# Kernel optimization log

Hardware: AMD Instinct MI355X
Metric: run time of the kernel (lower is better)

## Reference

```python
import jax, jax.numpy as jnp
import numpy as np

N, E, F_IN, OUT = 10000, 80000, 128, 32
H1, C1 = 8, 256   # conv1: heads=8, out_channels=256, concat=True
H2, C2 = 1, OUT   # conv2: heads=1, out_channels=OUT, concat=False
NEG_SLOPE = 0.2


def _add_self_loops(edge_index, edge_attr, n_nodes):
    # PyG fill_value='mean': self-loop edge_attr = mean of incoming edge attrs per dst node
    src, dst = edge_index[0], edge_index[1]
    s = jax.ops.segment_sum(edge_attr, dst, num_segments=n_nodes)
    cnt = jax.ops.segment_sum(jnp.ones((edge_attr.shape[0],), edge_attr.dtype), dst, num_segments=n_nodes)
    self_attr = s / jnp.maximum(cnt, 1.0)[:, None]
    loop = jnp.arange(n_nodes)
    return (jnp.concatenate([src, loop]), jnp.concatenate([dst, loop]),
            jnp.concatenate([edge_attr, self_attr], axis=0))


def _gatv2(x, src, dst, edge_attr, Wl, bl, Wr, br, We, att, bias, heads, out_ch, concat, n_nodes):
    xl = (x @ Wl + bl).reshape(n_nodes, heads, out_ch)   # source-side projection
    xr = (x @ Wr + br).reshape(n_nodes, heads, out_ch)   # target-side projection
    e = (edge_attr @ We).reshape(-1, heads, out_ch)      # edge feature projection (no bias in PyG)
    m = jax.nn.leaky_relu(xl[src] + xr[dst] + e, NEG_SLOPE)   # [Etot, H, C]
    logits = jnp.einsum('ehc,hc->eh', m, att)            # per-edge attention logits
    # segment softmax over edges grouped by destination node (stable)
    lmax = jax.ops.segment_max(logits, dst, num_segments=n_nodes)
    ex = jnp.exp(logits - lmax[dst])
    denom = jax.ops.segment_sum(ex, dst, num_segments=n_nodes)
    alpha = ex / denom[dst]                              # [Etot, H]
    out = jax.ops.segment_sum(xl[src] * alpha[:, :, None], dst, num_segments=n_nodes)  # [N, H, C]
    out = out.reshape(n_nodes, heads * out_ch) if concat else out.mean(axis=1)
    return out + bias


def setup_inputs() -> dict:
    key = jax.random.key(0)
    ks = jax.random.split(key, 17)
    s = 0.05
    return {
        'x': jax.random.normal(ks[0], (N, F_IN), jnp.float32),
        'edge_index': jax.random.randint(ks[1], (2, E), 0, N),
        'edge_attr': jax.random.normal(ks[2], (E, F_IN), jnp.float32),
        # conv1 params
        'Wl1': jax.random.normal(ks[3], (F_IN, H1 * C1), jnp.float32) * s,
        'bl1': jnp.zeros((H1 * C1,), jnp.float32),
        'Wr1': jax.random.normal(ks[4], (F_IN, H1 * C1), jnp.float32) * s,
        'br1': jnp.zeros((H1 * C1,), jnp.float32),
        'We1': jax.random.normal(ks[5], (F_IN, H1 * C1), jnp.float32) * s,
        'att1': jax.random.normal(ks[6], (H1, C1), jnp.float32) * s,
        'b1': jnp.zeros((H1 * C1,), jnp.float32),
        # conv2 params (input dim = H1*C1 = 2048)
        'Wl2': jax.random.normal(ks[7], (H1 * C1, H2 * C2), jnp.float32) * s,
        'bl2': jnp.zeros((H2 * C2,), jnp.float32),
        'Wr2': jax.random.normal(ks[8], (H1 * C1, H2 * C2), jnp.float32) * s,
        'br2': jnp.zeros((H2 * C2,), jnp.float32),
        'We2': jax.random.normal(ks[9], (F_IN, H2 * C2), jnp.float32) * s,
        'att2': jax.random.normal(ks[10], (H2, C2), jnp.float32) * s,
        'b2': jnp.zeros((C2,), jnp.float32),
    }


def reference(x, edge_index, edge_attr, Wl1, bl1, Wr1, br1, We1, att1, b1,
              Wl2, bl2, Wr2, br2, We2, att2, b2):
    # mode='eval': all dropouts are identity
    src, dst, ea = _add_self_loops(edge_index, edge_attr, N)
    h = _gatv2(x, src, dst, ea, Wl1, bl1, Wr1, br1, We1, att1, b1, H1, C1, True, N)
    h = jax.nn.relu(h)
    out = _gatv2(h, src, dst, ea, Wl2, bl2, Wr2, br2, We2, att2, b2, H2, C2, False, N)
    return jax.nn.relu(out)
```

## Files before the change

kernel.cpp:

```cpp
#include <hip/hip_runtime.h>
#include <hip/hip_bf16.h>

#define N_NODES 10000
#define N_EDGES 80000
#define ETOT (N_EDGES + N_NODES)
#define FD 128
#define D1 2048
#define D2 32
#define NEG 0.2f

typedef __hip_bfloat16 bf16;
typedef __attribute__((ext_vector_type(8))) short short8;
typedef __attribute__((ext_vector_type(4))) short short4v;
typedef __attribute__((ext_vector_type(4))) float f32x4;

__device__ __forceinline__ bf16 f2b(float v){ return __float2bfloat16(v); }
__device__ __forceinline__ short f2bs(float v){ bf16 t=__float2bfloat16(v); return *(short*)&t; }
__device__ __forceinline__ float b2fs(short s){
    return __uint_as_float(((unsigned int)(unsigned short)s) << 16);
}

__global__ void k_deg(const int* __restrict__ ei, int* __restrict__ deg){
    int e = blockIdx.x*256 + threadIdx.x;
    if(e < N_EDGES) atomicAdd(&deg[ei[N_EDGES+e]], 1);
}

__global__ void k_scan(const int* __restrict__ deg, int* __restrict__ row_start){
    __shared__ int sdata[256];
    int tid = threadIdx.x;
    const int CH = 40;
    int base = tid*CH;
    int lsum = 0;
    for(int i=0;i<CH;i++){ int v=base+i; if(v<N_NODES) lsum += deg[v]+1; }
    sdata[tid]=lsum; __syncthreads();
    for(int off=1; off<256; off<<=1){
        int val = (tid>=off)? sdata[tid-off] : 0;
        __syncthreads();
        sdata[tid] += val;
        __syncthreads();
    }
    int run = (tid>0)? sdata[tid-1] : 0;
    for(int i=0;i<CH;i++){
        int v=base+i;
        if(v<=N_NODES){
            row_start[v]=run;
            if(v<N_NODES) run += deg[v]+1;
        }
    }
}

__global__ void k_fill(const int* __restrict__ ei, const int* __restrict__ row_start,
                       int* __restrict__ cursor, int* __restrict__ ecsr,
                       int* __restrict__ srcs, int* __restrict__ dsts){
    int e = blockIdx.x*256 + threadIdx.x;
    if(e >= ETOT) return;
    int src = (e < N_EDGES) ? ei[e]          : (e - N_EDGES);
    int dst = (e < N_EDGES) ? ei[N_EDGES+e]  : (e - N_EDGES);
    int p = atomicAdd(&cursor[dst], 1);
    int pos = row_start[dst]+p;
    ecsr[pos] = e;
    srcs[pos] = src;
    dsts[pos] = dst;
}

__global__ void k_selfmean(const int* __restrict__ ecsr, const int* __restrict__ row_start,
                           const float* __restrict__ ea, float* __restrict__ self_attr){
    int v = blockIdx.x, t = threadIdx.x;
    int start=row_start[v], end=row_start[v+1];
    float s=0.f; int cnt=0;
    for(int i=start;i<end;i++){
        int e=ecsr[i];
        if(e<N_EDGES){ s += ea[(size_t)e*FD+t]; cnt++; }
    }
    self_attr[(size_t)v*FD+t] = s / fmaxf((float)cnt, 1.f);
}

__global__ void k_packAll(const float* __restrict__ We1, const float* __restrict__ Wl1,
                          const float* __restrict__ Wr1, const float* __restrict__ Wl2,
                          const float* __restrict__ Wr2, const float* __restrict__ We2,
                          short* __restrict__ Wb1, short* __restrict__ Wbl1,
                          short* __restrict__ Wbr1, short* __restrict__ Wb2,
                          short* __restrict__ Wb2e){
    int y = blockIdx.y;
    int idx = blockIdx.x*256 + threadIdx.x;
    if(y < 3){
        const float* W = (y==0)? We1 : (y==1)? Wl1 : Wr1;
        short* Wb      = (y==0)? Wb1 : (y==1)? Wbl1 : Wbr1;
        int k = idx >> 11, c = idx & 2047;
        int cb = c>>4, col = c&15, kc = k>>5, quad = (k>>3)&3, j = k&7;
        Wb[((size_t)(cb*4+kc)*64 + quad*16 + col)*8 + j] = f2bs(W[idx]);
    } else {
        if(idx < 131072){
            int k = idx >> 6, c = idx & 63;
            float v = (c < 32) ? Wl2[k*32 + c] : Wr2[k*32 + (c-32)];
            int cb = c>>4, col = c&15, kc = k>>5, quad = (k>>3)&3, j = k&7;
            Wb2[((size_t)(cb*64+kc)*64 + quad*16 + col)*8 + j] = f2bs(v);
        } else if(idx < 131072+4096){
            int t = idx - 131072;
            int k = t >> 5, c = t & 31;
            int cb = c>>4, col = c&15, kc = k>>5, quad = (k>>3)&3, j = k&7;
            Wb2e[((size_t)(cb*4+kc)*64 + quad*16 + col)*8 + j] = f2bs(We2[t]);
        }
    }
}

__global__ __launch_bounds__(256) void k_gemm1m(const float* __restrict__ x,
        const short* __restrict__ Wbl, const float* __restrict__ bl, bf16* __restrict__ outl,
        const short* __restrict__ Wbr, const float* __restrict__ br, bf16* __restrict__ outr){
    const short* Wb   = (blockIdx.y==0)? Wbl : Wbr;
    const float* bias = (blockIdx.y==0)? bl  : br;
    bf16* outp        = (blockIdx.y==0)? outl: outr;
    __shared__ short a_lds[32*128];
    __shared__ float tile[4][32][20];
    int tid = threadIdx.x;
    int r0 = blockIdx.x*32;
    for(int q=tid; q<32*128; q+=256){
        int m=q>>7, k=q&127;
        int gr=r0+m;
        float v = (gr<N_NODES)? x[(size_t)gr*FD+k] : 0.f;
        int kc=k>>5, quad=(k>>3)&3, j=k&7;
        a_lds[((kc*4+quad)*32+m)*8+j] = f2bs(v);
    }
    __syncthreads();
    int w=tid>>6, lane=tid&63, quad=lane>>4, col=lane&15;
    int arow=lane&31, half=lane>>5;
    short8 af[2][4];
    #pragma unroll
    for(int mg=0;mg<2;mg++)
        #pragma unroll
        for(int kc=0;kc<4;kc++)
            af[mg][kc] = *(const short8*)&a_lds[((kc*4+quad)*32+mg*16+col)*8];
    int orow = r0 + arow;
    for(int cbl=0;cbl<32;cbl++){
        int cbg = w*32+cbl;
        f32x4 c0={0,0,0,0}, c1={0,0,0,0};
        #pragma unroll
        for(int kc=0;kc<4;kc++){
            short8 bfr = *(const short8*)(Wb + ((size_t)(cbg*4+kc)*64 + lane)*8);
            c0 = __builtin_amdgcn_mfma_f32_16x16x32_bf16(af[0][kc], bfr, c0, 0,0,0);
            c1 = __builtin_amdgcn_mfma_f32_16x16x32_bf16(af[1][kc], bfr, c1, 0,0,0);
        }
        #pragma unroll
        for(int rg=0;rg<4;rg++){
            tile[w][quad*4+rg][col]    = c0[rg];
            tile[w][16+quad*4+rg][col] = c1[rg];
        }
        int cg = cbg*16 + half*8;
        float4 t0 = *(float4*)&tile[w][arow][half*8];
        float4 t1 = *(float4*)&tile[w][arow][half*8+4];
        float4 b0 = *(const float4*)(bias+cg);
        float4 b1v = *(const float4*)(bias+cg+4);
        if(orow < N_NODES){
            float tv[8]={t0.x,t0.y,t0.z,t0.w,t1.x,t1.y,t1.z,t1.w};
            float bb[8]={b0.x,b0.y,b0.z,b0.w,b1v.x,b1v.y,b1v.z,b1v.w};
            short8 ov;
            #pragma unroll
            for(int j=0;j<8;j++) ov[j] = f2bs(tv[j]+bb[j]);
            *(short8*)(outp + (size_t)orow*D1 + cg) = ov;
        }
    }
}

__global__ __launch_bounds__(256) void k_logit1(const int* __restrict__ ecsr,
        const int* __restrict__ srcs, const int* __restrict__ dsts,
        const float* __restrict__ ea, const float* __restrict__ self_attr,
        const bf16* __restrict__ xl1, const bf16* __restrict__ xr1,
        const short* __restrict__ Wb, const short* __restrict__ Wb2e,
        const float* __restrict__ att1,
        float* __restrict__ logits1p, float* __restrict__ e2){
    __shared__ short a_lds[64*128];
    __shared__ float tile[4][32][20];
    __shared__ int ssrc[64], sdst[64], sed[64];
    int tid = threadIdx.x;
    int i0 = blockIdx.x*64;
    if(tid<64){
        int i=i0+tid; if(i>=ETOT) i=ETOT-1;
        sed[tid]=ecsr[i]; ssrc[tid]=srcs[i]; sdst[tid]=dsts[i];
    }
    __syncthreads();
    for(int q=tid; q<64*32; q+=256){
        int m=q>>5, kq=(q&31)*4;
        int e=sed[m];
        const float* sp = (e<N_EDGES)? (ea+(size_t)e*FD+kq) : (self_attr+(size_t)(e-N_EDGES)*FD+kq);
        float4 v4 = *(const float4*)sp;
        int kc=kq>>5, quad=(kq>>3)&3, j=kq&7;
        short4v sv; sv[0]=f2bs(v4.x); sv[1]=f2bs(v4.y); sv[2]=f2bs(v4.z); sv[3]=f2bs(v4.w);
        *(short4v*)&a_lds[((kc*4+quad)*64+m)*8+j] = sv;
    }
    __syncthreads();
    int w=tid>>6, lane=tid&63, quad=lane>>4, col=lane&15;
    int arow=lane&31, half=lane>>5;
    short8 af[4][4];
    #pragma unroll
    for(int mg=0;mg<4;mg++)
        #pragma unroll
        for(int kc=0;kc<4;kc++)
            af[mg][kc] = *(const short8*)&a_lds[((kc*4+quad)*64+mg*16+col)*8];
    const bf16* xlpA = xl1 + (size_t)ssrc[arow]*D1;
    const bf16* xrpA = xr1 + (size_t)sdst[arow]*D1;
    const bf16* xlpB = xl1 + (size_t)ssrc[32+arow]*D1;
    const bf16* xrpB = xr1 + (size_t)sdst[32+arow]*D1;
    float acch[4]={0.f,0.f,0.f,0.f};
    for(int cbl=0;cbl<32;cbl++){
        int cbg = w*32+cbl;
        f32x4 c0={0,0,0,0}, c1={0,0,0,0}, c2={0,0,0,0}, c3={0,0,0,0};
        #pragma unroll
        for(int kc=0;kc<4;kc++){
            short8 bfr = *(const short8*)(Wb + ((size_t)(cbg*4+kc)*64 + lane)*8);
            c0 = __builtin_amdgcn_mfma_f32_16x16x32_bf16(af[0][kc], bfr, c0, 0,0,0);
            c1 = __builtin_amdgcn_mfma_f32_16x16x32_bf16(af[1][kc], bfr, c1, 0,0,0);
            c2 = __builtin_amdgcn_mfma_f32_16x16x32_bf16(af[2][kc], bfr, c2, 0,0,0);
            c3 = __builtin_amdgcn_mfma_f32_16x16x32_bf16(af[3][kc], bfr, c3, 0,0,0);
        }
        int hs = cbl>>4;
        int cg = cbg*16 + half*8;
        float4 a0 = *(const float4*)(att1+cg);
        float4 a1 = *(const float4*)(att1+cg+4);
        float av[8]={a0.x,a0.y,a0.z,a0.w,a1.x,a1.y,a1.z,a1.w};
        #pragma unroll
        for(int rg=0;rg<4;rg++){
            tile[w][quad*4+rg][col]    = c0[rg];
            tile[w][16+quad*4+rg][col] = c1[rg];
        }
        {
            float4 t0 = *(float4*)&tile[w][arow][half*8];
            float4 t1 = *(float4*)&tile[w][arow][half*8+4];
            short8 xlv = *(const short8*)(xlpA + cg);
            short8 xrv = *(const short8*)(xrpA + cg);
            float tv[8]={t0.x,t0.y,t0.z,t0.w,t1.x,t1.y,t1.z,t1.w};
            float acc = acch[hs];
            #pragma unroll
            for(int j=0;j<8;j++){
                float m = tv[j] + b2fs(xlv[j]) + b2fs(xrv[j]);
                m = (m>0.f)? m : NEG*m;
                acc += av[j]*m;
            }
            acch[hs] = acc;
        }
        #pragma unroll
        for(int rg=0;rg<4;rg++){
            tile[w][quad*4+rg][col]    = c2[rg];
            tile[w][16+quad*4+rg][col] = c3[rg];
        }
        {
            float4 t0 = *(float4*)&tile[w][arow][half*8];
            float4 t1 = *(float4*)&tile[w][arow][half*8+4];
            short8 xlv = *(const short8*)(xlpB + cg);
            short8 xrv = *(const short8*)(xrpB + cg);
            float tv[8]={t0.x,t0.y,t0.z,t0.w,t1.x,t1.y,t1.z,t1.w};
            float acc = acch[2+hs];
            #pragma unroll
            for(int j=0;j<8;j++){
                float m = tv[j] + b2fs(xlv[j]) + b2fs(xrv[j]);
                m = (m>0.f)? m : NEG*m;
                acc += av[j]*m;
            }
            acch[2+hs] = acc;
        }
    }
    if(w<2){
        f32x4 c0={0,0,0,0}, c1={0,0,0,0}, c2={0,0,0,0}, c3={0,0,0,0};
        #pragma unroll
        for(int kc=0;kc<4;kc++){
            short8 bfr = *(const short8*)(Wb2e + ((size_t)(w*4+kc)*64 + lane)*8);
            c0 = __builtin_amdgcn_mfma_f32_16x16x32_bf16(af[0][kc], bfr, c0, 0,0,0);
            c1 = __builtin_amdgcn_mfma_f32_16x16x32_bf16(af[1][kc], bfr, c1, 0,0,0);
            c2 = __builtin_amdgcn_mfma_f32_16x16x32_bf16(af[2][kc], bfr, c2, 0,0,0);
            c3 = __builtin_amdgcn_mfma_f32_16x16x32_bf16(af[3][kc], bfr, c3, 0,0,0);
        }
        #pragma unroll
        for(int rg=0;rg<4;rg++){
            tile[w][quad*4+rg][col]    = c0[rg];
            tile[w][16+quad*4+rg][col] = c1[rg];
        }
        {
            int i=i0+arow;
            float4 t0 = *(float4*)&tile[w][arow][half*8];
            float4 t1 = *(float4*)&tile[w][arow][half*8+4];
            if(i<ETOT){
                *(float4*)(e2 + (size_t)i*32 + w*16 + half*8)     = t0;
                *(float4*)(e2 + (size_t)i*32 + w*16 + half*8 + 4) = t1;
            }
        }
        #pragma unroll
        for(int rg=0;rg<4;rg++){
            tile[w][quad*4+rg][col]    = c2[rg];
            tile[w][16+quad*4+rg][col] = c3[rg];
        }
        {
            int i=i0+32+arow;
            float4 t0 = *(float4*)&tile[w][arow][half*8];
            float4 t1 = *(float4*)&tile[w][arow][half*8+4];
            if(i<ETOT){
                *(float4*)(e2 + (size_t)i*32 + w*16 + half*8)     = t0;
                *(float4*)(e2 + (size_t)i*32 + w*16 + half*8 + 4) = t1;
            }
        }
    }
    #pragma unroll
    for(int r=0;r<4;r++) acch[r] += __shfl_xor(acch[r],32);
    if(lane<32){
        int iA=i0+arow;
        if(iA<ETOT){
            logits1p[(size_t)iA*8 + w*2  ] = acch[0];
            logits1p[(size_t)iA*8 + w*2+1] = acch[1];
        }
        int iB=i0+32+arow;
        if(iB<ETOT){
            logits1p[(size_t)iB*8 + w*2  ] = acch[2];
            logits1p[(size_t)iB*8 + w*2+1] = acch[3];
        }
    }
}

__global__ void k_agg1(const int* __restrict__ srcs, const int* __restrict__ row_start,
                       const float* __restrict__ logits1p, const bf16* __restrict__ xl1,
                       const float* __restrict__ b1, bf16* __restrict__ hb){
    __shared__ float dden[8];
    __shared__ float salpha[32][8];
    int tid=threadIdx.x, v=blockIdx.x;
    int start=row_start[v], end=row_start[v+1];
    if(tid<8) dden[tid]=0.f;
    __syncthreads();
    float ds[8]={0,0,0,0,0,0,0,0};
    for(int i=start+tid;i<end;i+=256){
        const float* lp = logits1p+(size_t)i*8;
        float4 l0=*(const float4*)lp, l1=*(const float4*)(lp+4);
        ds[0]+=__expf(l0.x); ds[1]+=__expf(l0.y); ds[2]+=__expf(l0.z); ds[3]+=__expf(l0.w);
        ds[4]+=__expf(l1.x); ds[5]+=__expf(l1.y); ds[6]+=__expf(l1.z); ds[7]+=__expf(l1.w);
    }
    #pragma unroll
    for(int j=0;j<8;j++){
        float val=ds[j];
        #pragma unroll
        for(int off=32;off>=1;off>>=1) val += __shfl_down(val,off);
        if((tid&63)==0) atomicAdd(&dden[j], val);
    }
    __syncthreads();
    float rden[8];
    #pragma unroll
    for(int j=0;j<8;j++) rden[j]=1.f/dden[j];
    int myc = tid*8;
    int hj  = tid>>5;
    float acc[8]={0,0,0,0,0,0,0,0};
    for(int base=start; base<end; base+=32){
        int nle = end-base; if(nle>32) nle=32;
        __syncthreads();
        if(tid < nle*8){
            int le=tid>>3, j=tid&7;
            salpha[le][j] = __expf(logits1p[(size_t)(base+le)*8+j])*rden[j];
        }
        __syncthreads();
        for(int le=0; le<nle; le++){
            int src=srcs[base+le];
            short8 xv = *(const short8*)(xl1 + (size_t)src*D1 + myc);
            float al = salpha[le][hj];
            #pragma unroll
            for(int j=0;j<8;j++) acc[j] += al*b2fs(xv[j]);
        }
    }
    float4 bb0=*(const float4*)(b1+myc), bb1=*(const float4*)(b1+myc+4);
    float bv[8]={bb0.x,bb0.y,bb0.z,bb0.w,bb1.x,bb1.y,bb1.z,bb1.w};
    short8 ov;
    #pragma unroll
    for(int j=0;j<8;j++) ov[j] = f2bs(fmaxf(acc[j]+bv[j],0.f));
    *(short8*)(hb + (size_t)v*D1 + myc) = ov;
}

__global__ __launch_bounds__(256) void k_gemm2(const bf16* __restrict__ hb,
        const short* __restrict__ Wb2, const float* __restrict__ bl2,
        const float* __restrict__ br2, float* __restrict__ xl2, float* __restrict__ xr2){
    __shared__ float cacc[4][16][64];
    int tid=threadIdx.x, w=tid>>6, lane=tid&63, quad=lane>>4, col=lane&15;
    int r0 = blockIdx.x*16;
    const bf16* hp = hb + (size_t)(r0+col)*D1 + quad*8;
    f32x4 acc[4] = {{0,0,0,0},{0,0,0,0},{0,0,0,0},{0,0,0,0}};
    for(int kc=w*16; kc<w*16+16; kc++){
        short8 af = *(const short8*)(hp + kc*32);
        #pragma unroll
        for(int cb=0;cb<4;cb++){
            short8 bfr = *(const short8*)(Wb2 + ((size_t)(cb*64+kc)*64 + lane)*8);
            acc[cb] = __builtin_amdgcn_mfma_f32_16x16x32_bf16(af, bfr, acc[cb], 0,0,0);
        }
    }
    #pragma unroll
    for(int cb=0;cb<4;cb++)
        #pragma unroll
        for(int rg=0;rg<4;rg++)
            cacc[w][quad*4+rg][cb*16+col] = acc[cb][rg];
    __syncthreads();
    #pragma unroll
    for(int i=0;i<4;i++){
        int idx = tid + 256*i;
        int r = idx>>6, c = idx&63;
        float s = cacc[0][r][c]+cacc[1][r][c]+cacc[2][r][c]+cacc[3][r][c];
        int rr = r0 + r;
        if(c<32) xl2[rr*32+c]      = s + bl2[c];
        else     xr2[rr*32+(c-32)] = s + br2[c-32];
    }
}

__global__ void k_agg2f(const int* __restrict__ srcs, const int* __restrict__ row_start,
                        const float* __restrict__ e2, const float* __restrict__ xl2,
                        const float* __restrict__ xr2, const float* __restrict__ att2,
                        const float* __restrict__ b2v, float* __restrict__ out){
    int tid=threadIdx.x, v=blockIdx.x;
    int start=row_start[v], end=row_start[v+1];
    int le=tid>>5, c=tid&31;
    float xr2v = xr2[v*32+c];
    float attc = att2[c];
    float ds=0.f;
    for(int i=start+le;i<end;i+=2){
        int src=srcs[i];
        float m = e2[(size_t)i*32+c] + xl2[src*32+c] + xr2v;
        m = fmaxf(m, NEG*m);
        float p = attc*m;
        #pragma unroll
        for(int off=16;off>=1;off>>=1) p += __shfl_down(p,off,32);
        p = __shfl(p, 0, 32);
        ds += __expf(p);
    }
    ds += __shfl_xor(ds,32);
    float rden = 1.f/ds;
    float acc=0.f;
    for(int i=start+le;i<end;i+=2){
        int src=srcs[i];
        float xlv = xl2[src*32+c];
        float m = e2[(size_t)i*32+c] + xlv + xr2v;
        m = fmaxf(m, NEG*m);
        float p = attc*m;
        #pragma unroll
        for(int off=16;off>=1;off>>=1) p += __shfl_down(p,off,32);
        p = __shfl(p, 0, 32);
        acc += __expf(p)*rden*xlv;
    }
    acc += __shfl_xor(acc,32);
    if(tid<32) out[(size_t)v*D2+c] = fmaxf(acc + b2v[c], 0.f);
}

extern "C" void kernel_launch(void* const* d_in, const int* in_sizes, int n_in,
                              void* d_out, int out_size, void* d_ws, size_t ws_size,
                              hipStream_t stream) {
    const float* x    = (const float*)d_in[0];
    const int*   ei   = (const int*)d_in[1];
    const float* ea   = (const float*)d_in[2];
    const float* Wl1  = (const float*)d_in[3];
    const float* bl1  = (const float*)d_in[4];
    const float* Wr1  = (const float*)d_in[5];
    const float* br1  = (const float*)d_in[6];
    const float* We1  = (const float*)d_in[7];
    const float* att1 = (const float*)d_in[8];
    const float* b1   = (const float*)d_in[9];
    const float* Wl2  = (const float*)d_in[10];
    const float* bl2  = (const float*)d_in[11];
    const float* Wr2  = (const float*)d_in[12];
    const float* br2  = (const float*)d_in[13];
    const float* We2  = (const float*)d_in[14];
    const float* att2 = (const float*)d_in[15];
    const float* b2v  = (const float*)d_in[16];
    float* out = (float*)d_out;

    char* ws = (char*)d_ws;
    size_t off = 0;
    auto alloc = [&](size_t bytes)->char* {
        char* p = ws + off;
        off += (bytes + 255) & ~(size_t)255;
        return p;
    };
    float* self_attr = (float*)alloc((size_t)N_NODES*FD*4);
    int*   deg       = (int*)  alloc((size_t)N_NODES*4);
    int*   cursor    = (int*)  alloc((size_t)N_NODES*4);
    int*   row_start = (int*)  alloc((size_t)(N_NODES+1)*4);
    int*   ecsr      = (int*)  alloc((size_t)ETOT*4);
    int*   srcs      = (int*)  alloc((size_t)ETOT*4);
    int*   dsts      = (int*)  alloc((size_t)ETOT*4);
    float* logits1p  = (float*)alloc((size_t)ETOT*8*4);
    float* e2        = (float*)alloc((size_t)ETOT*32*4);
    bf16*  xl1       = (bf16*) alloc((size_t)N_NODES*D1*2);
    bf16*  xr1       = (bf16*) alloc((size_t)N_NODES*D1*2);
    bf16*  hb        = (bf16*) alloc((size_t)N_NODES*D1*2);
    float* xl2       = (float*)alloc((size_t)N_NODES*D2*4);
    float* xr2       = (float*)alloc((size_t)N_NODES*D2*4);
    short* Wb1       = (short*)alloc((size_t)FD*D1*2);
    short* Wbl1      = (short*)alloc((size_t)FD*D1*2);
    short* Wbr1      = (short*)alloc((size_t)FD*D1*2);
    short* Wb2       = (short*)alloc((size_t)D1*64*2);
    short* Wb2e      = (short*)alloc((size_t)FD*D2*2);
    (void)ws_size; (void)in_sizes; (void)n_in; (void)out_size;

    hipMemsetAsync(deg,    0, (size_t)N_NODES*4, stream);
    hipMemsetAsync(cursor, 0, (size_t)N_NODES*4, stream);

    k_deg<<<(N_EDGES+255)/256, 256, 0, stream>>>(ei, deg);
    k_scan<<<1, 256, 0, stream>>>(deg, row_start);
    k_fill<<<(ETOT+255)/256, 256, 0, stream>>>(ei, row_start, cursor, ecsr, srcs, dsts);
    k_selfmean<<<N_NODES, 128, 0, stream>>>(ecsr, row_start, ea, self_attr);
    dim3 gp(1024, 4);
    k_packAll<<<gp, 256, 0, stream>>>(We1, Wl1, Wr1, Wl2, Wr2, We2,
                                      Wb1, Wbl1, Wbr1, Wb2, Wb2e);

    dim3 g1((N_NODES+31)/32, 2);
    k_gemm1m<<<g1, 256, 0, stream>>>(x, Wbl1, bl1, xl1, Wbr1, br1, xr1);

    k_logit1<<<(ETOT+63)/64, 256, 0, stream>>>(ecsr, srcs, dsts, ea, self_attr,
                                               xl1, xr1, Wb1, Wb2e, att1, logits1p, e2);
    k_agg1<<<N_NODES, 256, 0, stream>>>(srcs, row_start, logits1p, xl1, b1, hb);

    k_gemm2<<<N_NODES/16, 256, 0, stream>>>(hb, Wb2, bl2, br2, xl2, xr2);
    k_agg2f<<<N_NODES, 64, 0, stream>>>(srcs, row_start, e2, xl2, xr2, att2, b2v, out);
}
```

Measured before the change: 437.2 us.

## Remove block syncs in agg1, fuse softmax pass in agg2, alias logit tile

In k_agg1, each wavefront now computes the softmax denominators for its own two heads with wave shuffles and computes the alpha of each edge inline. This replaces the LDS atomics, the shared alpha staging and the per-chunk __syncthreads. In k_agg2f, the denominator and the weighted sum are accumulated in one pass and divided at the end, so the gathers no longer run twice. In k_logit1, the epilogue tile now aliases the A-operand LDS buffer after an added barrier, which cuts shared memory per block and may raise occupancy. The cost is a redundant expf per edge per wave in agg1 and no max-subtraction in the single-pass agg2 accumulation.

```diff
diff --git a/kernel.cpp b/kernel.cpp
--- a/kernel.cpp
+++ b/kernel.cpp
@@ -169,8 +169,8 @@
         const float* __restrict__ att1,
         float* __restrict__ logits1p, float* __restrict__ e2){
     __shared__ short a_lds[64*128];
-    __shared__ float tile[4][32][20];
     __shared__ int ssrc[64], sdst[64], sed[64];
+    float (*tile)[32][20] = reinterpret_cast<float(*)[32][20]>(a_lds);
     int tid = threadIdx.x;
     int i0 = blockIdx.x*64;
     if(tid<64){
@@ -196,6 +196,7 @@
         #pragma unroll
         for(int kc=0;kc<4;kc++)
             af[mg][kc] = *(const short8*)&a_lds[((kc*4+quad)*64+mg*16+col)*8];
+    __syncthreads();
     const bf16* xlpA = xl1 + (size_t)ssrc[arow]*D1;
     const bf16* xrpA = xr1 + (size_t)sdst[arow]*D1;
     const bf16* xlpB = xl1 + (size_t)ssrc[32+arow]*D1;
@@ -316,48 +317,31 @@
 __global__ void k_agg1(const int* __restrict__ srcs, const int* __restrict__ row_start,
                        const float* __restrict__ logits1p, const bf16* __restrict__ xl1,
                        const float* __restrict__ b1, bf16* __restrict__ hb){
-    __shared__ float dden[8];
-    __shared__ float salpha[32][8];
     int tid=threadIdx.x, v=blockIdx.x;
     int start=row_start[v], end=row_start[v+1];
-    if(tid<8) dden[tid]=0.f;
-    __syncthreads();
-    float ds[8]={0,0,0,0,0,0,0,0};
-    for(int i=start+tid;i<end;i+=256){
-        const float* lp = logits1p+(size_t)i*8;
-        float4 l0=*(const float4*)lp, l1=*(const float4*)(lp+4);
-        ds[0]+=__expf(l0.x); ds[1]+=__expf(l0.y); ds[2]+=__expf(l0.z); ds[3]+=__expf(l0.w);
-        ds[4]+=__expf(l1.x); ds[5]+=__expf(l1.y); ds[6]+=__expf(l1.z); ds[7]+=__expf(l1.w);
-    }
-    #pragma unroll
-    for(int j=0;j<8;j++){
-        float val=ds[j];
-        #pragma unroll
-        for(int off=32;off>=1;off>>=1) val += __shfl_down(val,off);
-        if((tid&63)==0) atomicAdd(&dden[j], val);
-    }
-    __syncthreads();
-    float rden[8];
-    #pragma unroll
-    for(int j=0;j<8;j++) rden[j]=1.f/dden[j];
-    int myc = tid*8;
-    int hj  = tid>>5;
+    int w=tid>>6, lane=tid&63;
+    int hpar = lane>>5;
+    int myc = w*512 + lane*8;
+    float ds0=0.f, ds1=0.f;
+    for(int i=start+lane;i<end;i+=64){
+        float2 lg = *(const float2*)(logits1p + (size_t)i*8 + w*2);
+        ds0 += __expf(lg.x);
+        ds1 += __expf(lg.y);
+    }
+    #pragma unroll
+    for(int off=32;off>=1;off>>=1){
+        ds0 += __shfl_xor(ds0,off);
+        ds1 += __shfl_xor(ds1,off);
+    }
+    float rden = 1.f/((hpar==0)? ds0 : ds1);
     float acc[8]={0,0,0,0,0,0,0,0};
-    for(int base=start; base<end; base+=32){
-        int nle = end-base; if(nle>32) nle=32;
-        __syncthreads();
-        if(tid < nle*8){
-            int le=tid>>3, j=tid&7;
-            salpha[le][j] = __expf(logits1p[(size_t)(base+le)*8+j])*rden[j];
-        }
-        __syncthreads();
-        for(int le=0; le<nle; le++){
-            int src=srcs[base+le];
-            short8 xv = *(const short8*)(xl1 + (size_t)src*D1 + myc);
-            float al = salpha[le][hj];
-            #pragma unroll
-            for(int j=0;j<8;j++) acc[j] += al*b2fs(xv[j]);
-        }
+    for(int i=start;i<end;i++){
+        int src = srcs[i];
+        float2 lg = *(const float2*)(logits1p + (size_t)i*8 + w*2);
+        float al = __expf((hpar==0)? lg.x : lg.y) * rden;
+        short8 xv = *(const short8*)(xl1 + (size_t)src*D1 + myc);
+        #pragma unroll
+        for(int j=0;j<8;j++) acc[j] += al*b2fs(xv[j]);
     }
     float4 bb0=*(const float4*)(b1+myc), bb1=*(const float4*)(b1+myc+4);
     float bv[8]={bb0.x,bb0.y,bb0.z,bb0.w,bb1.x,bb1.y,bb1.z,bb1.w};
@@ -409,20 +393,7 @@
     int le=tid>>5, c=tid&31;
     float xr2v = xr2[v*32+c];
     float attc = att2[c];
-    float ds=0.f;
-    for(int i=start+le;i<end;i+=2){
-        int src=srcs[i];
-        float m = e2[(size_t)i*32+c] + xl2[src*32+c] + xr2v;
-        m = fmaxf(m, NEG*m);
-        float p = attc*m;
-        #pragma unroll
-        for(int off=16;off>=1;off>>=1) p += __shfl_down(p,off,32);
-        p = __shfl(p, 0, 32);
-        ds += __expf(p);
-    }
-    ds += __shfl_xor(ds,32);
-    float rden = 1.f/ds;
-    float acc=0.f;
+    float ds=0.f, acc=0.f;
     for(int i=start+le;i<end;i+=2){
         int src=srcs[i];
         float xlv = xl2[src*32+c];
@@ -432,10 +403,13 @@
         #pragma unroll
         for(int off=16;off>=1;off>>=1) p += __shfl_down(p,off,32);
         p = __shfl(p, 0, 32);
-        acc += __expf(p)*rden*xlv;
-    }
+        float ep = __expf(p);
+        ds  += ep;
+        acc += ep*xlv;
+    }
+    ds  += __shfl_xor(ds,32);
     acc += __shfl_xor(acc,32);
-    if(tid<32) out[(size_t)v*D2+c] = fmaxf(acc + b2v[c], 0.f);
+    if(tid<32) out[(size_t)v*D2+c] = fmaxf(acc/ds + b2v[c], 0.f);
 }
 
 extern "C" void kernel_launch(void* const* d_in, const int* in_sizes, int n_in,
```

After: 426.9 us. -2.3%, faster.
